# Kernel tuning notes

Hardware: AMD Instinct MI355X
Metric: run time of the kernel (lower is better)

Reference implementation:

```python
import jax, jax.numpy as jnp
import numpy as np

N_NODES = 100000
N_EDGES = 3200000
N_GRAPHS = 4096
BN_EPS = 1e-5


def setup_inputs() -> dict:
    key = jax.random.key(0)
    ks = iter(jax.random.split(key, 64))
    d = {}
    d["x"] = jax.random.normal(next(ks), (N_NODES, 36), dtype=jnp.float32)
    d["edge_index"] = jax.random.randint(next(ks), (2, N_EDGES), 0, N_NODES, dtype=jnp.int32)
    d["batch"] = jnp.sort(jax.random.randint(next(ks), (N_NODES,), 0, N_GRAPHS, dtype=jnp.int32))
    d["num_graphs"] = N_GRAPHS
    # GCN layers: (in, out) per hidden_dims=[128,128,64]
    dims = [(36, 128), (128, 128), (128, 64)]
    for i, (di, do) in enumerate(dims):
        d[f"w{i}"] = jax.random.normal(next(ks), (di, do), dtype=jnp.float32) * (1.0 / np.sqrt(di))
        d[f"b{i}"] = jax.random.normal(next(ks), (do,), dtype=jnp.float32) * 0.01
        d[f"g{i}"] = jax.random.uniform(next(ks), (do,), dtype=jnp.float32, minval=0.5, maxval=1.5)
        d[f"be{i}"] = jax.random.normal(next(ks), (do,), dtype=jnp.float32) * 0.01
        d[f"m{i}"] = jax.random.normal(next(ks), (do,), dtype=jnp.float32) * 0.01
        d[f"v{i}"] = jax.random.uniform(next(ks), (do,), dtype=jnp.float32, minval=0.5, maxval=1.5)
    # FC head: 64 -> 128 -> 64 -> 2
    d["fw0"] = jax.random.normal(next(ks), (64, 128), dtype=jnp.float32) * (1.0 / 8.0)
    d["fb0"] = jax.random.normal(next(ks), (128,), dtype=jnp.float32) * 0.01
    d["fw1"] = jax.random.normal(next(ks), (128, 64), dtype=jnp.float32) * (1.0 / np.sqrt(128))
    d["fb1"] = jax.random.normal(next(ks), (64,), dtype=jnp.float32) * 0.01
    d["ow"] = jax.random.normal(next(ks), (64, 2), dtype=jnp.float32) * (1.0 / 8.0)
    d["ob"] = jax.random.normal(next(ks), (2,), dtype=jnp.float32) * 0.01
    return d


def _gcn_layer(x, w, b, src, dst, norm_e, norm_self, n_nodes):
    # PyG GCNConv with self-loops: out[i] = sum_j norm_ij * (x_j @ W) + b
    xw = x @ w                                   # [N, out]
    msg = xw[src] * norm_e[:, None]              # gather + scale, [E, out]
    agg = jax.ops.segment_sum(msg, dst, num_segments=n_nodes)
    return agg + xw * norm_self[:, None] + b     # self-loop contribution + bias


def _bn_eval(x, g, be, m, v):
    return g * (x - m) * jax.lax.rsqrt(v + BN_EPS) + be


def reference(x, edge_index, batch, num_graphs,
              w0, b0, g0, be0, m0, v0,
              w1, b1, g1, be1, m1, v1,
              w2, b2, g2, be2, m2, v2,
              fw0, fb0, fw1, fb1, ow, ob):
    n = x.shape[0]
    src, dst = edge_index[0], edge_index[1]
    # symmetric GCN normalization with self-loops (gcn_norm)
    deg = jax.ops.segment_sum(jnp.ones(src.shape[0], x.dtype), dst, num_segments=n) + 1.0
    dinv = jax.lax.rsqrt(deg)
    norm_e = dinv[src] * dinv[dst]   # per-edge coeff
    norm_self = dinv * dinv          # self-loop coeff = 1/deg

    params = [(w0, b0, g0, be0, m0, v0), (w1, b1, g1, be1, m1, v1), (w2, b2, g2, be2, m2, v2)]
    h = x
    for (w, b, g, be, m, v) in params:
        h = _gcn_layer(h, w, b, src, dst, norm_e, norm_self, n)
        h = jax.nn.relu(_bn_eval(h, g, be, m, v))  # dropout inactive in eval

    # global mean pool over graphs
    sums = jax.ops.segment_sum(h, batch, num_segments=num_graphs)          # [G, 64]
    cnt = jax.ops.segment_sum(jnp.ones(n, h.dtype), batch, num_segments=num_graphs)
    pooled = sums / jnp.maximum(cnt, 1.0)[:, None]

    h = jax.nn.relu(pooled @ fw0 + fb0)
    h = jax.nn.relu(h @ fw1 + fb1)
    return h @ ow + ob
```

## Files before the change

kernel.cpp:

```cpp
#include <hip/hip_runtime.h>
#include <hip/hip_fp16.h>

#define BN_EPS 1e-5f

#define BUCK_SHIFT 9
#define NBUCK_MAX 256
#define BCAP 20480
#define PBLK 512

__global__ __launch_bounds__(256) void fused_scatter(const int* __restrict__ src,
                                                     const int* __restrict__ dst,
                                                     int* __restrict__ gcnt,
                                                     int2* __restrict__ ebuf,
                                                     int nE, int nbuck, int chunk) {
    __shared__ int h[NBUCK_MAX], rbase[NBUCK_MAX], cur[NBUCK_MAX];
    const int blk = blockIdx.x, tid = threadIdx.x;
    for (int j = tid; j < nbuck; j += 256) { h[j] = 0; cur[j] = 0; }
    __syncthreads();
    const int base = blk * chunk;
    const int end = min(base + chunk, nE);
    for (int i = base + tid; i < end; i += 256)
        atomicAdd(&h[dst[i] >> BUCK_SHIFT], 1);
    __syncthreads();
    for (int j = tid; j < nbuck; j += 256)
        rbase[j] = h[j] ? atomicAdd(&gcnt[j], h[j]) : 0;
    __syncthreads();
    for (int i = base + tid; i < end; i += 256) {
        int s = src[i], d = dst[i];
        int b = d >> BUCK_SHIFT;
        int p = rbase[b] + atomicAdd(&cur[b], 1);
        if (p < BCAP) ebuf[(size_t)b * BCAP + p] = make_int2(s, d);
    }
}

__global__ __launch_bounds__(256) void fused_csr(const int2* __restrict__ ebuf,
                                                 const int* __restrict__ gcnt,
                                                 const float* __restrict__ x,
                                                 const int* __restrict__ batch,
                                                 int* __restrict__ degI,
                                                 float* __restrict__ dinv,
                                                 int* __restrict__ row_start,
                                                 int* __restrict__ src_sorted,
                                                 __half* __restrict__ xs_h,
                                                 float* __restrict__ cnt, int n) {
    __shared__ int deg[512];
    __shared__ int cur[512];
    __shared__ float sdi[512];
    __shared__ int tmp[256];
    __shared__ int s_low_total;
    const int b = blockIdx.x, tid = threadIdx.x;
    const int nb = b << BUCK_SHIFT;
    const int cntb = min(gcnt[b], BCAP);
    const int2* __restrict__ eb = ebuf + (size_t)b * BCAP;

    for (int j = tid; j < 512; j += 256) deg[j] = 0;
    __syncthreads();
    for (int i = tid; i < cntb; i += 256)
        atomicAdd(&deg[eb[i].y - nb], 1);
    __syncthreads();

    for (int j = tid; j < 512; j += 256) {
        int node = nb + j;
        if (node < n) {
            int d = deg[j];
            degI[node] = d;
            float di = rsqrtf((float)d + 1.0f);
            dinv[node] = di;
            sdi[j] = di;
        }
    }

    int v0 = deg[tid];
    tmp[tid] = v0;
    __syncthreads();
    for (int off = 1; off < 256; off <<= 1) {
        int t = (tid >= off) ? tmp[tid - off] : 0;
        __syncthreads();
        tmp[tid] += t;
        __syncthreads();
    }
    int ex_low = tmp[tid] - v0;
    if (tid == 255) s_low_total = tmp[255];
    __syncthreads();
    int low_total = s_low_total;
    int v1 = deg[256 + tid];
    __syncthreads();
    tmp[tid] = v1;
    __syncthreads();
    for (int off = 1; off < 256; off <<= 1) {
        int t = (tid >= off) ? tmp[tid - off] : 0;
        __syncthreads();
        tmp[tid] += t;
        __syncthreads();
    }
    int ex_high = tmp[tid] - v1 + low_total;

    const int gbase = b * BCAP;
    if (nb + tid < n) row_start[nb + tid] = gbase + ex_low;
    if (nb + 256 + tid < n) row_start[nb + 256 + tid] = gbase + ex_high;
    cur[tid] = ex_low;
    cur[256 + tid] = ex_high;
    __syncthreads();

    for (int i = tid; i < cntb; i += 256) {
        int2 ed = eb[i];
        int p = atomicAdd(&cur[ed.y - nb], 1);
        src_sorted[gbase + p] = ed.x;
    }

    for (int idx = tid; idx < 512 * 18; idx += 256) {
        int j = idx / 18;
        int node = nb + j;
        if (node < n) {
            int c = idx - j * 18;
            float2 v = *(const float2*)(x + (size_t)node * 36 + 2 * c);
            float di = sdi[j];
            *(__half2*)(xs_h + (size_t)node * 36 + 2 * c) = __floats2half2_rn(v.x * di, v.y * di);
        }
    }

    for (int j = tid; j < 512; j += 256) {
        int node = nb + j;
        if (node < n) unsafeAtomicAdd(&cnt[batch[node]], 1.0f);
    }
}

__global__ __launch_bounds__(256) void agg_pull36w_h(const __half* __restrict__ xs_h,
                                                     const int* __restrict__ row_start,
                                                     const int* __restrict__ degI,
                                                     const int* __restrict__ src_sorted,
                                                     const float* __restrict__ dinv,
                                                     float* __restrict__ out, int n) {
    int node = __builtin_amdgcn_readfirstlane((int)(blockIdx.x * 4 + (threadIdx.x >> 6)));
    if (node >= n) return;
    const int lane = threadIdx.x & 63;
    int e = row_start[node];
    const int re = e + degI[node];
    const float di = dinv[node];

    const char* __restrict__ xb = (const char*)xs_h;
    const unsigned loff = (unsigned)lane << 2;

    float2 acc = make_float2(0.f, 0.f);
    if (lane < 18) acc = __half22float2(*(const __half2*)(xb + ((unsigned)node * 72u + loff)));

    for (; e + 3 < re; e += 4) {
        int s0 = src_sorted[e], s1 = src_sorted[e + 1],
            s2 = src_sorted[e + 2], s3 = src_sorted[e + 3];
        if (lane < 18) {
            float2 a0 = __half22float2(*(const __half2*)(xb + ((unsigned)s0 * 72u + loff)));
            float2 a1 = __half22float2(*(const __half2*)(xb + ((unsigned)s1 * 72u + loff)));
            float2 a2 = __half22float2(*(const __half2*)(xb + ((unsigned)s2 * 72u + loff)));
            float2 a3 = __half22float2(*(const __half2*)(xb + ((unsigned)s3 * 72u + loff)));
            acc.x += (a0.x + a1.x) + (a2.x + a3.x);
            acc.y += (a0.y + a1.y) + (a2.y + a3.y);
        }
    }
    for (; e < re; e++) {
        int s = src_sorted[e];
        if (lane < 18) {
            float2 a = __half22float2(*(const __half2*)(xb + ((unsigned)s * 72u + loff)));
            acc.x += a.x;
            acc.y += a.y;
        }
    }
    if (lane < 18) {
        float2 o;
        o.x = acc.x * di;
        o.y = acc.y * di;
        *(float2*)(out + (size_t)node * 36 + 2 * lane) = o;
    }
}

__global__ __launch_bounds__(256) void agg_pull_wave2_h(const __half* __restrict__ feat_h,
                                                        const int* __restrict__ row_start,
                                                        const int* __restrict__ degI,
                                                        const int* __restrict__ src_sorted,
                                                        const float* __restrict__ dinv,
                                                        __half* __restrict__ out, int n) {
    int node = __builtin_amdgcn_readfirstlane((int)(blockIdx.x * 4 + (threadIdx.x >> 6)));
    if (node >= n) return;
    const int lane = threadIdx.x & 63;
    int e = row_start[node];
    const int re = e + degI[node];
    const float di = dinv[node];

    const char* __restrict__ fb = (const char*)feat_h;
    const unsigned loff = (unsigned)lane << 2;

    float2 acc = __half22float2(*(const __half2*)(fb + (((unsigned)node << 8) + loff)));

    for (; e + 3 < re; e += 4) {
        int s0 = src_sorted[e], s1 = src_sorted[e + 1],
            s2 = src_sorted[e + 2], s3 = src_sorted[e + 3];
        float2 a0 = __half22float2(*(const __half2*)(fb + (((unsigned)s0 << 8) + loff)));
        float2 a1 = __half22float2(*(const __half2*)(fb + (((unsigned)s1 << 8) + loff)));
        float2 a2 = __half22float2(*(const __half2*)(fb + (((unsigned)s2 << 8) + loff)));
        float2 a3 = __half22float2(*(const __half2*)(fb + (((unsigned)s3 << 8) + loff)));
        acc.x += (a0.x + a1.x) + (a2.x + a3.x);
        acc.y += (a0.y + a1.y) + (a2.y + a3.y);
    }
    for (; e < re; e++) {
        int s = src_sorted[e];
        float2 a = __half22float2(*(const __half2*)(fb + (((unsigned)s << 8) + loff)));
        acc.x += a.x;
        acc.y += a.y;
    }
    __half2 o = __floats2half2_rn(acc.x * di, acc.y * di);
    *(__half2*)((char*)out + (((unsigned)node << 8) + loff)) = o;
}

template<int IN, int OUT, bool BNRELU, bool SCALEOUT, bool OUTHALF>
__global__ __launch_bounds__(256) void gemm_rt(const float* __restrict__ in,
                                               const float* __restrict__ W,
                                               const float* __restrict__ bias,
                                               const float* __restrict__ gg,
                                               const float* __restrict__ bb,
                                               const float* __restrict__ mm,
                                               const float* __restrict__ vv,
                                               const float* __restrict__ dscale,
                                               void* __restrict__ outp, int n) {
    constexpr int BM = 64;
    constexpr int TN = 8;
    constexpr int CG = OUT / TN;
    constexpr int RG = 256 / CG;
    constexpr int TM = BM / RG;
    constexpr int PAD = (IN == 36) ? 8 : 4;
    constexpr int LDW = IN + PAD;
    __shared__ float s_a[BM][LDW];

    const int r0 = blockIdx.x * BM;
    const int tid = threadIdx.x;

    constexpr int T4 = BM * IN / 4;
    for (int i4 = tid; i4 < T4; i4 += 256) {
        int idx = i4 * 4;
        int r = idx / IN;
        int k = idx - r * IN;
        int row = r0 + r;
        float4 v = make_float4(0.f, 0.f, 0.f, 0.f);
        if (row < n) v = *(const float4*)(in + (size_t)row * IN + k);
        *(float4*)&s_a[r][k] = v;
    }
    __syncthreads();

    const int tx = tid % CG;
    const int ty = tid / CG;
    const int c0 = tx * TN;
    const int rr = ty * TM;

    float acc[TM][TN];
#pragma unroll
    for (int j = 0; j < TM; j++)
#pragma unroll
        for (int t = 0; t < TN; t++) acc[j][t] = 0.0f;

#pragma unroll 2
    for (int k = 0; k < IN; k += 4) {
        float4 a[TM];
#pragma unroll
        for (int j = 0; j < TM; j++) a[j] = *(const float4*)&s_a[rr + j][k];
#pragma unroll
        for (int kk = 0; kk < 4; kk++) {
            float4 wv0 = *(const float4*)(W + (size_t)(k + kk) * OUT + c0);
            float4 wv1 = *(const float4*)(W + (size_t)(k + kk) * OUT + c0 + 4);
#pragma unroll
            for (int j = 0; j < TM; j++) {
                float av = (kk == 0) ? a[j].x : (kk == 1) ? a[j].y : (kk == 2) ? a[j].z : a[j].w;
                acc[j][0] += av * wv0.x;
                acc[j][1] += av * wv0.y;
                acc[j][2] += av * wv0.z;
                acc[j][3] += av * wv0.w;
                acc[j][4] += av * wv1.x;
                acc[j][5] += av * wv1.y;
                acc[j][6] += av * wv1.z;
                acc[j][7] += av * wv1.w;
            }
        }
    }

    float scl[TN], sft[TN];
    if constexpr (BNRELU) {
#pragma unroll
        for (int t = 0; t < TN; t++) {
            float s = gg[c0 + t] * rsqrtf(vv[c0 + t] + BN_EPS);
            scl[t] = s;
            sft[t] = bb[c0 + t] + (bias[c0 + t] - mm[c0 + t]) * s;
        }
    }

#pragma unroll
    for (int j = 0; j < TM; j++) {
        int row = r0 + rr + j;
        if (row < n) {
            float ds = 1.0f;
            if constexpr (SCALEOUT) ds = dscale[row];
            float o[TN];
#pragma unroll
            for (int t = 0; t < TN; t++) {
                float val = acc[j][t];
                if constexpr (BNRELU) val = fmaxf(val * scl[t] + sft[t], 0.0f);
                if constexpr (SCALEOUT) val *= ds;
                o[t] = val;
            }
            if constexpr (OUTHALF) {
                union { __half h[8]; float4 v; } u;
#pragma unroll
                for (int t = 0; t < TN; t++) u.h[t] = __float2half_rn(o[t]);
                *(float4*)((char*)outp + ((size_t)row * OUT + c0) * 2) = u.v;
            } else {
                float* op = (float*)outp + (size_t)row * OUT + c0;
                *(float4*)op = make_float4(o[0], o[1], o[2], o[3]);
                *(float4*)(op + 4) = make_float4(o[4], o[5], o[6], o[7]);
            }
        }
    }
}

__global__ __launch_bounds__(256) void gemm12(const __half* __restrict__ inA,
                                              const float* __restrict__ W1,
                                              const float* __restrict__ b1,
                                              const float* __restrict__ g1,
                                              const float* __restrict__ be1,
                                              const float* __restrict__ m1,
                                              const float* __restrict__ v1,
                                              const float* __restrict__ W2,
                                              const float* __restrict__ dscale,
                                              __half* __restrict__ out, int n) {
    __shared__ __half s_a[64][136];
    __shared__ float  s_h[64][132];
    const int r0 = blockIdx.x * 64;
    const int tid = threadIdx.x;

    for (int i8 = tid; i8 < 1024; i8 += 256) {
        int idx = i8 * 8;
        int r = idx >> 7;
        int k = idx & 127;
        int row = r0 + r;
        uint4 v = make_uint4(0u, 0u, 0u, 0u);
        if (row < n) v = *(const uint4*)(inA + (size_t)row * 128 + k);
        *(uint4*)&s_a[r][k] = v;
    }
    __syncthreads();

    {
        const int tx = tid & 15, ty = tid >> 4;
        const int c0 = tx * 8, rr = ty * 4;
        float acc[4][8];
#pragma unroll
        for (int j = 0; j < 4; j++)
#pragma unroll
            for (int t = 0; t < 8; t++) acc[j][t] = 0.0f;

#pragma unroll 2
        for (int k = 0; k < 128; k += 4) {
            float a[4][4];
#pragma unroll
            for (int j = 0; j < 4; j++) {
                float2 f0 = __half22float2(*(const __half2*)&s_a[rr + j][k]);
                float2 f1 = __half22float2(*(const __half2*)&s_a[rr + j][k + 2]);
                a[j][0] = f0.x; a[j][1] = f0.y; a[j][2] = f1.x; a[j][3] = f1.y;
            }
#pragma unroll
            for (int kk = 0; kk < 4; kk++) {
                float4 wv0 = *(const float4*)(W1 + (size_t)(k + kk) * 128 + c0);
                float4 wv1 = *(const float4*)(W1 + (size_t)(k + kk) * 128 + c0 + 4);
#pragma unroll
                for (int j = 0; j < 4; j++) {
                    float av = a[j][kk];
                    acc[j][0] += av * wv0.x;
                    acc[j][1] += av * wv0.y;
                    acc[j][2] += av * wv0.z;
                    acc[j][3] += av * wv0.w;
                    acc[j][4] += av * wv1.x;
                    acc[j][5] += av * wv1.y;
                    acc[j][6] += av * wv1.z;
                    acc[j][7] += av * wv1.w;
                }
            }
        }
        float scl[8], sft[8];
#pragma unroll
        for (int t = 0; t < 8; t++) {
            float s = g1[c0 + t] * rsqrtf(v1[c0 + t] + BN_EPS);
            scl[t] = s;
            sft[t] = be1[c0 + t] + (b1[c0 + t] - m1[c0 + t]) * s;
        }
#pragma unroll
        for (int j = 0; j < 4; j++) {
            float4 o0, o1;
            o0.x = fmaxf(acc[j][0] * scl[0] + sft[0], 0.f);
            o0.y = fmaxf(acc[j][1] * scl[1] + sft[1], 0.f);
            o0.z = fmaxf(acc[j][2] * scl[2] + sft[2], 0.f);
            o0.w = fmaxf(acc[j][3] * scl[3] + sft[3], 0.f);
            o1.x = fmaxf(acc[j][4] * scl[4] + sft[4], 0.f);
            o1.y = fmaxf(acc[j][5] * scl[5] + sft[5], 0.f);
            o1.z = fmaxf(acc[j][6] * scl[6] + sft[6], 0.f);
            o1.w = fmaxf(acc[j][7] * scl[7] + sft[7], 0.f);
            *(float4*)&s_h[rr + j][c0] = o0;
            *(float4*)&s_h[rr + j][c0 + 4] = o1;
        }
    }
    __syncthreads();

    {
        const int tx = tid & 7, ty = tid >> 3;
        const int c0 = tx * 8, rr = ty * 2;
        float acc[2][8];
#pragma unroll
        for (int j = 0; j < 2; j++)
#pragma unroll
            for (int t = 0; t < 8; t++) acc[j][t] = 0.0f;

#pragma unroll 2
        for (int k = 0; k < 128; k += 4) {
            float4 a0 = *(const float4*)&s_h[rr][k];
            float4 a1 = *(const float4*)&s_h[rr + 1][k];
#pragma unroll
            for (int kk = 0; kk < 4; kk++) {
                float4 wv0 = *(const float4*)(W2 + (size_t)(k + kk) * 64 + c0);
                float4 wv1 = *(const float4*)(W2 + (size_t)(k + kk) * 64 + c0 + 4);
                float av0 = (kk == 0) ? a0.x : (kk == 1) ? a0.y : (kk == 2) ? a0.z : a0.w;
                float av1 = (kk == 0) ? a1.x : (kk == 1) ? a1.y : (kk == 2) ? a1.z : a1.w;
                acc[0][0] += av0 * wv0.x; acc[0][1] += av0 * wv0.y;
                acc[0][2] += av0 * wv0.z; acc[0][3] += av0 * wv0.w;
                acc[0][4] += av0 * wv1.x; acc[0][5] += av0 * wv1.y;
                acc[0][6] += av0 * wv1.z; acc[0][7] += av0 * wv1.w;
                acc[1][0] += av1 * wv0.x; acc[1][1] += av1 * wv0.y;
                acc[1][2] += av1 * wv0.z; acc[1][3] += av1 * wv0.w;
                acc[1][4] += av1 * wv1.x; acc[1][5] += av1 * wv1.y;
                acc[1][6] += av1 * wv1.z; acc[1][7] += av1 * wv1.w;
            }
        }
#pragma unroll
        for (int j = 0; j < 2; j++) {
            int row = r0 + rr + j;
            if (row < n) {
                float ds = dscale[row];
                union { __half h[8]; uint4 v; } u;
#pragma unroll
                for (int t = 0; t < 8; t++) u.h[t] = __float2half_rn(acc[j][t] * ds);
                *(uint4*)(out + (size_t)row * 64 + c0) = u.v;
            }
        }
    }
}

__global__ __launch_bounds__(256) void agg_pull_pool_h(const __half* __restrict__ feat_h,
                                                       const int* __restrict__ row_start,
                                                       const int* __restrict__ degI,
                                                       const int* __restrict__ src_sorted,
                                                       const float* __restrict__ dinv,
                                                       const float* __restrict__ bias,
                                                       const float* __restrict__ gg,
                                                       const float* __restrict__ bb,
                                                       const float* __restrict__ mm,
                                                       const float* __restrict__ vv,
                                                       const int* __restrict__ batch,
                                                       float* __restrict__ pool, int n) {
    int node = __builtin_amdgcn_readfirstlane((int)(blockIdx.x * 4 + (threadIdx.x >> 6)));
    if (node >= n) return;
    const int lane = threadIdx.x & 63;
    int e = row_start[node];
    const int re = e + degI[node];
    const float di = dinv[node];

    const char* __restrict__ fb = (const char*)feat_h;
    const unsigned loff = (unsigned)lane << 1;

    float acc = __half2float(*(const __half*)(fb + (((unsigned)node << 7) + loff)));

    for (; e + 3 < re; e += 4) {
        int s0 = src_sorted[e], s1 = src_sorted[e + 1],
            s2 = src_sorted[e + 2], s3 = src_sorted[e + 3];
        float a0 = __half2float(*(const __half*)(fb + (((unsigned)s0 << 7) + loff)));
        float a1 = __half2float(*(const __half*)(fb + (((unsigned)s1 << 7) + loff)));
        float a2 = __half2float(*(const __half*)(fb + (((unsigned)s2 << 7) + loff)));
        float a3 = __half2float(*(const __half*)(fb + (((unsigned)s3 << 7) + loff)));
        acc += (a0 + a1) + (a2 + a3);
    }
    for (; e < re; e++) {
        acc += __half2float(*(const __half*)(fb + (((unsigned)src_sorted[e] << 7) + loff)));
    }
    float h = acc * di + bias[lane];
    float scale = gg[lane] * rsqrtf(vv[lane] + BN_EPS);
    float val = fmaxf((h - mm[lane]) * scale + bb[lane], 0.0f);
    unsafeAtomicAdd(&pool[(size_t)batch[node] * 64 + lane], val);
}

__global__ __launch_bounds__(128) void fc_head_kernel(const float* __restrict__ pool,
                                                      const float* __restrict__ cnt,
                                                      const float* __restrict__ fw0,
                                                      const float* __restrict__ fb0,
                                                      const float* __restrict__ fw1,
                                                      const float* __restrict__ fb1,
                                                      const float* __restrict__ ow,
                                                      const float* __restrict__ ob,
                                                      float* __restrict__ out) {
    int g = blockIdx.x, tid = threadIdx.x;
    __shared__ float p[64], h1[128], h2[64];
    if (tid < 64) p[tid] = pool[g * 64 + tid] / fmaxf(cnt[g], 1.0f);
    __syncthreads();
    {
        float acc = fb0[tid];
        for (int k = 0; k < 64; k++) acc += p[k] * fw0[k * 128 + tid];
        h1[tid] = fmaxf(acc, 0.0f);
    }
    __syncthreads();
    if (tid < 64) {
        float acc = fb1[tid];
        for (int k = 0; k < 128; k++) acc += h1[k] * fw1[k * 64 + tid];
        h2[tid] = fmaxf(acc, 0.0f);
    }
    __syncthreads();
    if (tid < 2) {
        float acc = ob[tid];
        for (int k = 0; k < 64; k++) acc += h2[k] * ow[k * 2 + tid];
        out[g * 2 + tid] = acc;
    }
}

extern "C" void kernel_launch(void* const* d_in, const int* in_sizes, int n_in,
                              void* d_out, int out_size, void* d_ws, size_t ws_size,
                              hipStream_t stream) {
    const float* x     = (const float*)d_in[0];
    const int*   eidx  = (const int*)d_in[1];
    const int*   batch = (const int*)d_in[2];
    const float* w0 = (const float*)d_in[4];
    const float* b0 = (const float*)d_in[5];
    const float* g0 = (const float*)d_in[6];
    const float* be0 = (const float*)d_in[7];
    const float* m0 = (const float*)d_in[8];
    const float* v0 = (const float*)d_in[9];
    const float* w1 = (const float*)d_in[10];
    const float* b1 = (const float*)d_in[11];
    const float* g1 = (const float*)d_in[12];
    const float* be1 = (const float*)d_in[13];
    const float* m1 = (const float*)d_in[14];
    const float* v1 = (const float*)d_in[15];
    const float* w2 = (const float*)d_in[16];
    const float* b2 = (const float*)d_in[17];
    const float* g2 = (const float*)d_in[18];
    const float* be2 = (const float*)d_in[19];
    const float* m2 = (const float*)d_in[20];
    const float* v2 = (const float*)d_in[21];
    const float* fw0 = (const float*)d_in[22];
    const float* fb0 = (const float*)d_in[23];
    const float* fw1 = (const float*)d_in[24];
    const float* fb1 = (const float*)d_in[25];
    const float* ow = (const float*)d_in[26];
    const float* ob = (const float*)d_in[27];

    const int N = in_sizes[0] / 36;
    const int E = in_sizes[1] / 2;
    const int G = out_size / 2;
    const int* src = eidx;
    const int* dst = eidx + E;

    const int nbuck = (N + 511) >> BUCK_SHIFT;
    const int chunk = (E + PBLK - 1) / PBLK;

    char* wsb = (char*)d_ws;
    int2*   ebuf       = (int2*)wsb;    wsb += (size_t)nbuck * BCAP * 8;
    __half* F1         = (__half*)wsb;  wsb += (size_t)N * 128 * 2;
    __half* F1a        = (__half*)wsb;  wsb += (size_t)N * 128 * 2;
    __half* F2         = (__half*)wsb;  wsb += (size_t)N * 64 * 2;
    float*  A36        = (float*)wsb;   wsb += (size_t)N * 36 * 4;
    __half* xs_h       = (__half*)wsb;  wsb += (size_t)N * 36 * 2;
    int*    src_sorted = (int*)wsb;     wsb += (size_t)nbuck * BCAP * 4;
    int*    degI       = (int*)wsb;     wsb += (size_t)N * 4;
    int*    row_start  = (int*)wsb;     wsb += (size_t)N * 4;
    float*  dinv       = (float*)wsb;   wsb += (size_t)N * 4;
    float*  pool       = (float*)wsb;   wsb += (size_t)G * 64 * 4;
    float*  cnt        = (float*)wsb;   wsb += (size_t)G * 4;
    int*    gcnt       = (int*)wsb;     wsb += 256 * 4;

    hipMemsetAsync(gcnt, 0, 256 * 4, stream);
    hipMemsetAsync(pool, 0, (size_t)G * 64 * 4, stream);
    hipMemsetAsync(cnt, 0, (size_t)G * 4, stream);

    fused_scatter<<<PBLK, 256, 0, stream>>>(src, dst, gcnt, ebuf, E, nbuck, chunk);
    fused_csr<<<nbuck, 256, 0, stream>>>(ebuf, gcnt, x, batch, degI, dinv, row_start,
                                         src_sorted, xs_h, cnt, N);

    const int NW = (N + 3) / 4;
    const int NG = (N + 63) / 64;

    agg_pull36w_h<<<NW, 256, 0, stream>>>(xs_h, row_start, degI, src_sorted, dinv, A36, N);
    gemm_rt<36, 128, true, true, true><<<NG, 256, 0, stream>>>(
        A36, w0, b0, g0, be0, m0, v0, dinv, (void*)F1, N);

    agg_pull_wave2_h<<<NW, 256, 0, stream>>>(F1, row_start, degI, src_sorted, dinv, F1a, N);
    gemm12<<<NG, 256, 0, stream>>>(F1a, w1, b1, g1, be1, m1, v1, w2, dinv, F2, N);

    agg_pull_pool_h<<<NW, 256, 0, stream>>>(
        F2, row_start, degI, src_sorted, dinv, b2, g2, be2, m2, v2, batch, pool, N);

    fc_head_kernel<<<G, 128, 0, stream>>>(pool, cnt, fw0, fb0, fw1, fb1, ow, ob, (float*)d_out);
}
```

Measured before the change: 649.6 us.

## Store layer-0 aggregate in fp16 and split fused gemm12 into two generic GEMMs

The 36-wide aggregation now writes fp16 instead of fp32, and the first GEMM reads fp16 input, which halves that intermediate's traffic. The fused layer-1/layer-2 GEMM kernel is replaced by two launches of a generic half-input GEMM template. The intermediate 128-wide activation goes through an fp16 buffer that reuses the edge-bucket workspace. This drops the large combined shared-memory footprint of gemm12, which may raise occupancy. In exchange it adds an extra global round trip, an extra launch, and more fp16 rounding.

```diff
diff --git a/kernel.cpp b/kernel.cpp
--- a/kernel.cpp
+++ b/kernel.cpp
@@ -130,7 +130,7 @@
                                                      const int* __restrict__ degI,
                                                      const int* __restrict__ src_sorted,
                                                      const float* __restrict__ dinv,
-                                                     float* __restrict__ out, int n) {
+                                                     __half* __restrict__ out, int n) {
     int node = __builtin_amdgcn_readfirstlane((int)(blockIdx.x * 4 + (threadIdx.x >> 6)));
     if (node >= n) return;
     const int lane = threadIdx.x & 63;
@@ -165,10 +165,8 @@
         }
     }
     if (lane < 18) {
-        float2 o;
-        o.x = acc.x * di;
-        o.y = acc.y * di;
-        *(float2*)(out + (size_t)node * 36 + 2 * lane) = o;
+        __half2 o = __floats2half2_rn(acc.x * di, acc.y * di);
+        *(__half2*)((char*)out + ((unsigned)node * 72u + loff)) = o;
     }
 }
 
@@ -210,16 +208,16 @@
     *(__half2*)((char*)out + (((unsigned)node << 8) + loff)) = o;
 }
 
-template<int IN, int OUT, bool BNRELU, bool SCALEOUT, bool OUTHALF>
-__global__ __launch_bounds__(256) void gemm_rt(const float* __restrict__ in,
-                                               const float* __restrict__ W,
-                                               const float* __restrict__ bias,
-                                               const float* __restrict__ gg,
-                                               const float* __restrict__ bb,
-                                               const float* __restrict__ mm,
-                                               const float* __restrict__ vv,
-                                               const float* __restrict__ dscale,
-                                               void* __restrict__ outp, int n) {
+template<int IN, int OUT, bool BNRELU, bool SCALEOUT>
+__global__ __launch_bounds__(256) void gemm_rth(const __half* __restrict__ in,
+                                                const float* __restrict__ W,
+                                                const float* __restrict__ bias,
+                                                const float* __restrict__ gg,
+                                                const float* __restrict__ bb,
+                                                const float* __restrict__ mm,
+                                                const float* __restrict__ vv,
+                                                const float* __restrict__ dscale,
+                                                __half* __restrict__ out, int n) {
     constexpr int BM = 64;
     constexpr int TN = 8;
     constexpr int CG = OUT / TN;
@@ -232,15 +230,34 @@
     const int r0 = blockIdx.x * BM;
     const int tid = threadIdx.x;
 
-    constexpr int T4 = BM * IN / 4;
-    for (int i4 = tid; i4 < T4; i4 += 256) {
-        int idx = i4 * 4;
-        int r = idx / IN;
-        int k = idx - r * IN;
-        int row = r0 + r;
-        float4 v = make_float4(0.f, 0.f, 0.f, 0.f);
-        if (row < n) v = *(const float4*)(in + (size_t)row * IN + k);
-        *(float4*)&s_a[r][k] = v;
+    if constexpr (IN == 128) {
+        for (int i8 = tid; i8 < BM * 16; i8 += 256) {
+            int idx = i8 * 8;
+            int r = idx >> 7;
+            int k = idx & 127;
+            int row = r0 + r;
+            uint4 v = make_uint4(0u, 0u, 0u, 0u);
+            if (row < n) v = *(const uint4*)(in + (size_t)row * 128 + k);
+            const __half2* hp = (const __half2*)&v;
+            float2 f0 = __half22float2(hp[0]);
+            float2 f1 = __half22float2(hp[1]);
+            float2 f2 = __half22float2(hp[2]);
+            float2 f3 = __half22float2(hp[3]);
+            *(float4*)&s_a[r][k]     = make_float4(f0.x, f0.y, f1.x, f1.y);
+            *(float4*)&s_a[r][k + 4] = make_float4(f2.x, f2.y, f3.x, f3.y);
+        }
+    } else {
+        for (int i2 = tid; i2 < BM * (IN / 2); i2 += 256) {
+            int r = i2 / (IN / 2);
+            int k = (i2 - r * (IN / 2)) * 2;
+            int row = r0 + r;
+            __half2 hv;
+            *(unsigned*)&hv = 0u;
+            if (row < n) hv = *(const __half2*)(in + (size_t)row * IN + k);
+            float2 f = __half22float2(hv);
+            s_a[r][k] = f.x;
+            s_a[r][k + 1] = f.y;
+        }
     }
     __syncthreads();
 
@@ -295,153 +312,15 @@
         if (row < n) {
             float ds = 1.0f;
             if constexpr (SCALEOUT) ds = dscale[row];
-            float o[TN];
+            union { __half h[8]; uint4 v; } u;
 #pragma unroll
             for (int t = 0; t < TN; t++) {
                 float val = acc[j][t];
                 if constexpr (BNRELU) val = fmaxf(val * scl[t] + sft[t], 0.0f);
                 if constexpr (SCALEOUT) val *= ds;
-                o[t] = val;
+                u.h[t] = __float2half_rn(val);
             }
-            if constexpr (OUTHALF) {
-                union { __half h[8]; float4 v; } u;
-#pragma unroll
-                for (int t = 0; t < TN; t++) u.h[t] = __float2half_rn(o[t]);
-                *(float4*)((char*)outp + ((size_t)row * OUT + c0) * 2) = u.v;
-            } else {
-                float* op = (float*)outp + (size_t)row * OUT + c0;
-                *(float4*)op = make_float4(o[0], o[1], o[2], o[3]);
-                *(float4*)(op + 4) = make_float4(o[4], o[5], o[6], o[7]);
-            }
-        }
-    }
-}
-
-__global__ __launch_bounds__(256) void gemm12(const __half* __restrict__ inA,
-                                              const float* __restrict__ W1,
-                                              const float* __restrict__ b1,
-                                              const float* __restrict__ g1,
-                                              const float* __restrict__ be1,
-                                              const float* __restrict__ m1,
-                                              const float* __restrict__ v1,
-                                              const float* __restrict__ W2,
-                                              const float* __restrict__ dscale,
-                                              __half* __restrict__ out, int n) {
-    __shared__ __half s_a[64][136];
-    __shared__ float  s_h[64][132];
-    const int r0 = blockIdx.x * 64;
-    const int tid = threadIdx.x;
-
-    for (int i8 = tid; i8 < 1024; i8 += 256) {
-        int idx = i8 * 8;
-        int r = idx >> 7;
-        int k = idx & 127;
-        int row = r0 + r;
-        uint4 v = make_uint4(0u, 0u, 0u, 0u);
-        if (row < n) v = *(const uint4*)(inA + (size_t)row * 128 + k);
-        *(uint4*)&s_a[r][k] = v;
-    }
-    __syncthreads();
-
-    {
-        const int tx = tid & 15, ty = tid >> 4;
-        const int c0 = tx * 8, rr = ty * 4;
-        float acc[4][8];
-#pragma unroll
-        for (int j = 0; j < 4; j++)
-#pragma unroll
-            for (int t = 0; t < 8; t++) acc[j][t] = 0.0f;
-
-#pragma unroll 2
-        for (int k = 0; k < 128; k += 4) {
-            float a[4][4];
-#pragma unroll
-            for (int j = 0; j < 4; j++) {
-                float2 f0 = __half22float2(*(const __half2*)&s_a[rr + j][k]);
-                float2 f1 = __half22float2(*(const __half2*)&s_a[rr + j][k + 2]);
-                a[j][0] = f0.x; a[j][1] = f0.y; a[j][2] = f1.x; a[j][3] = f1.y;
-            }
-#pragma unroll
-            for (int kk = 0; kk < 4; kk++) {
-                float4 wv0 = *(const float4*)(W1 + (size_t)(k + kk) * 128 + c0);
-                float4 wv1 = *(const float4*)(W1 + (size_t)(k + kk) * 128 + c0 + 4);
-#pragma unroll
-                for (int j = 0; j < 4; j++) {
-                    float av = a[j][kk];
-                    acc[j][0] += av * wv0.x;
-                    acc[j][1] += av * wv0.y;
-                    acc[j][2] += av * wv0.z;
-                    acc[j][3] += av * wv0.w;
-                    acc[j][4] += av * wv1.x;
-                    acc[j][5] += av * wv1.y;
-                    acc[j][6] += av * wv1.z;
-                    acc[j][7] += av * wv1.w;
-                }
-            }
-        }
-        float scl[8], sft[8];
-#pragma unroll
-        for (int t = 0; t < 8; t++) {
-            float s = g1[c0 + t] * rsqrtf(v1[c0 + t] + BN_EPS);
-            scl[t] = s;
-            sft[t] = be1[c0 + t] + (b1[c0 + t] - m1[c0 + t]) * s;
-        }
-#pragma unroll
-        for (int j = 0; j < 4; j++) {
-            float4 o0, o1;
-            o0.x = fmaxf(acc[j][0] * scl[0] + sft[0], 0.f);
-            o0.y = fmaxf(acc[j][1] * scl[1] + sft[1], 0.f);
-            o0.z = fmaxf(acc[j][2] * scl[2] + sft[2], 0.f);
-            o0.w = fmaxf(acc[j][3] * scl[3] + sft[3], 0.f);
-            o1.x = fmaxf(acc[j][4] * scl[4] + sft[4], 0.f);
-            o1.y = fmaxf(acc[j][5] * scl[5] + sft[5], 0.f);
-            o1.z = fmaxf(acc[j][6] * scl[6] + sft[6], 0.f);
-            o1.w = fmaxf(acc[j][7] * scl[7] + sft[7], 0.f);
-            *(float4*)&s_h[rr + j][c0] = o0;
-            *(float4*)&s_h[rr + j][c0 + 4] = o1;
-        }
-    }
-    __syncthreads();
-
-    {
-        const int tx = tid & 7, ty = tid >> 3;
-        const int c0 = tx * 8, rr = ty * 2;
-        float acc[2][8];
-#pragma unroll
-        for (int j = 0; j < 2; j++)
-#pragma unroll
-            for (int t = 0; t < 8; t++) acc[j][t] = 0.0f;
-
-#pragma unroll 2
-        for (int k = 0; k < 128; k += 4) {
-            float4 a0 = *(const float4*)&s_h[rr][k];
-            float4 a1 = *(const float4*)&s_h[rr + 1][k];
-#pragma unroll
-            for (int kk = 0; kk < 4; kk++) {
-                float4 wv0 = *(const float4*)(W2 + (size_t)(k + kk) * 64 + c0);
-                float4 wv1 = *(const float4*)(W2 + (size_t)(k + kk) * 64 + c0 + 4);
-                float av0 = (kk == 0) ? a0.x : (kk == 1) ? a0.y : (kk == 2) ? a0.z : a0.w;
-                float av1 = (kk == 0) ? a1.x : (kk == 1) ? a1.y : (kk == 2) ? a1.z : a1.w;
-                acc[0][0] += av0 * wv0.x; acc[0][1] += av0 * wv0.y;
-                acc[0][2] += av0 * wv0.z; acc[0][3] += av0 * wv0.w;
-                acc[0][4] += av0 * wv1.x; acc[0][5] += av0 * wv1.y;
-                acc[0][6] += av0 * wv1.z; acc[0][7] += av0 * wv1.w;
-                acc[1][0] += av1 * wv0.x; acc[1][1] += av1 * wv0.y;
-                acc[1][2] += av1 * wv0.z; acc[1][3] += av1 * wv0.w;
-                acc[1][4] += av1 * wv1.x; acc[1][5] += av1 * wv1.y;
-                acc[1][6] += av1 * wv1.z; acc[1][7] += av1 * wv1.w;
-            }
-        }
-#pragma unroll
-        for (int j = 0; j < 2; j++) {
-            int row = r0 + rr + j;
-            if (row < n) {
-                float ds = dscale[row];
-                union { __half h[8]; uint4 v; } u;
-#pragma unroll
-                for (int t = 0; t < 8; t++) u.h[t] = __float2half_rn(acc[j][t] * ds);
-                *(uint4*)(out + (size_t)row * 64 + c0) = u.v;
-            }
+            *(uint4*)(out + (size_t)row * OUT + c0) = u.v;
         }
     }
 }
@@ -565,7 +444,7 @@
     __half* F1         = (__half*)wsb;  wsb += (size_t)N * 128 * 2;
     __half* F1a        = (__half*)wsb;  wsb += (size_t)N * 128 * 2;
     __half* F2         = (__half*)wsb;  wsb += (size_t)N * 64 * 2;
-    float*  A36        = (float*)wsb;   wsb += (size_t)N * 36 * 4;
+    __half* A36h       = (__half*)wsb;  wsb += (size_t)N * 36 * 2;
     __half* xs_h       = (__half*)wsb;  wsb += (size_t)N * 36 * 2;
     int*    src_sorted = (int*)wsb;     wsb += (size_t)nbuck * BCAP * 4;
     int*    degI       = (int*)wsb;     wsb += (size_t)N * 4;
@@ -574,6 +453,7 @@
     float*  pool       = (float*)wsb;   wsb += (size_t)G * 64 * 4;
     float*  cnt        = (float*)wsb;   wsb += (size_t)G * 4;
     int*    gcnt       = (int*)wsb;     wsb += 256 * 4;
+    __half* F1b        = (__half*)ebuf;
 
     hipMemsetAsync(gcnt, 0, 256 * 4, stream);
     hipMemsetAsync(pool, 0, (size_t)G * 64 * 4, stream);
@@ -586,12 +466,16 @@
     const int NW = (N + 3) / 4;
     const int NG = (N + 63) / 64;
 
-    agg_pull36w_h<<<NW, 256, 0, stream>>>(xs_h, row_start, degI, src_sorted, dinv, A36, N);
-    gemm_rt<36, 128, true, true, true><<<NG, 256, 0, stream>>>(
-        A36, w0, b0, g0, be0, m0, v0, dinv, (void*)F1, N);
+    agg_pull36w_h<<<NW, 256, 0, stream>>>(xs_h, row_start, degI, src_sorted, dinv, A36h, N);
+    gemm_rth<36, 128, true, true><<<NG, 256, 0, stream>>>(
+        A36h, w0, b0, g0, be0, m0, v0, dinv, F1, N);
 
     agg_pull_wave2_h<<<NW, 256, 0, stream>>>(F1, row_start, degI, src_sorted, dinv, F1a, N);
-    gemm12<<<NG, 256, 0, stream>>>(F1a, w1, b1, g1, be1, m1, v1, w2, dinv, F2, N);
+    gemm_rth<128, 128, true, false><<<NG, 256, 0, stream>>>(
+        F1a, w1, b1, g1, be1, m1, v1, nullptr, F1b, N);
+
+    gemm_rth<128, 64, false, true><<<NG, 256, 0, stream>>>(
+        F1b, w2, nullptr, nullptr, nullptr, nullptr, nullptr, dinv, F2, N);
 
     agg_pull_pool_h<<<NW, 256, 0, stream>>>(
         F2, row_start, degI, src_sorted, dinv, b2, g2, be2, m2, v2, batch, pool, N);
```

Result: slower. 670.1 us (+3.2%).
